# Kernel tuning notes

Measured on AMD Instinct MI355X. Metric: run time of the kernel, lower is better.

## Reference

```python
import jax, jax.numpy as jnp
import numpy as np

H = 40  # HIDDEN_SIZE


def _gru_layer(x_tbi, Wih, Whh, bih, bhh):
    """PyTorch-convention GRU layer. x_tbi: (T, B, I). Returns (ys (T,B,H), h_T (B,H)).
    Gate order in stacked weights is (r, z, n) as in torch.nn.GRU:
      r = sigmoid(W_ir x + b_ir + W_hr h + b_hr)
      z = sigmoid(W_iz x + b_iz + W_hz h + b_hz)
      n = tanh(W_in x + b_in + r * (W_hn h + b_hn))
      h' = (1 - z) * n + z * h
    """
    # Precompute all input projections in one big GEMM: (T,B,3H)
    xg = jnp.einsum('tbi,gi->tbg', x_tbi, Wih) + bih
    B = x_tbi.shape[1]
    h0 = jnp.zeros((B, H), x_tbi.dtype)

    def step(h, xg_t):
        hg = h @ Whh.T + bhh                       # (B, 3H)
        xr, xz, xn = jnp.split(xg_t, 3, axis=-1)
        hr, hz, hn = jnp.split(hg, 3, axis=-1)
        r = jax.nn.sigmoid(xr + hr)
        z = jax.nn.sigmoid(xz + hz)
        n = jnp.tanh(xn + r * hn)
        h_new = (1.0 - z) * n + z * h
        return h_new, h_new

    hT, ys = jax.lax.scan(step, h0, xg)
    return ys, hT


def setup_inputs() -> dict:
    key = jax.random.key(0)
    ks = jax.random.split(key, 9)
    B, T, I = 4096, 256, 16
    s = 1.0 / np.sqrt(H)  # torch GRU init: U(-1/sqrt(H), 1/sqrt(H))
    u = lambda k, shape: jax.random.uniform(k, shape, jnp.float32, -s, s)
    return {
        "x": jax.random.normal(ks[0], (B, T, I), jnp.float32),
        "Wih0": u(ks[1], (3 * H, I)),
        "Whh0": u(ks[2], (3 * H, H)),
        "bih0": u(ks[3], (3 * H,)),
        "bhh0": u(ks[4], (3 * H,)),
        "Wih1": u(ks[5], (3 * H, H)),
        "Whh1": u(ks[6], (3 * H, H)),
        "bih1": u(ks[7], (3 * H,)),
        "bhh1": u(ks[8], (3 * H,)),
    }


def reference(x, Wih0, Whh0, bih0, bhh0, Wih1, Whh1, bih1, bhh1):
    # batch_first input (B,T,I) -> time-major (T,B,I) for scan
    x_tbi = jnp.transpose(x, (1, 0, 2))
    y0, _ = _gru_layer(x_tbi, Wih0, Whh0, bih0, bhh0)   # layer 0 full sequence
    _, hT = _gru_layer(y0, Wih1, Whh1, bih1, bhh1)      # layer 1 final state
    return hT  # (B, H) == h[-1]
```

## Files before the change

kernel.cpp:

```cpp
#include <hip/hip_runtime.h>

#define T_STEPS 256
#define HID 40
#define EPB 16
#define NTHR 640
#define RR 56
#define PP (16 * RR)
#define OL1 (2 * PP)
#define STOT (4 * PP)

typedef __attribute__((ext_vector_type(8))) short bf16x8;
typedef __attribute__((ext_vector_type(4))) float f32x4;
typedef __attribute__((ext_vector_type(8))) float f32x8;
typedef __attribute__((ext_vector_type(4))) unsigned int u32x4;

__device__ __forceinline__ unsigned short bf16_rne(float v) {
    unsigned int x = __float_as_uint(v);
    unsigned int r = x + 0x7FFFu + ((x >> 16) & 1u);
    return (unsigned short)(r >> 16);
}
__device__ __forceinline__ unsigned short bf16_cvt(float v) {
    unsigned int r;
    asm("v_cvt_pk_bf16_f32 %0, %1, %2" : "=v"(r) : "v"(v), "v"(v));
    return (unsigned short)r;
}
__device__ __forceinline__ float sigm(float v) {
    return __builtin_amdgcn_rcpf(1.0f + __builtin_amdgcn_exp2f(-1.4426950408889634f * v));
}
__device__ __forceinline__ float tanh_f(float v) {
    return 1.0f - 2.0f * __builtin_amdgcn_rcpf(__builtin_amdgcn_exp2f(2.8853900817779268f * v) + 1.0f);
}

#define MF(A_, B_, C_) C_ = __builtin_amdgcn_mfma_f32_16x16x32_bf16(A_, B_, C_, 0, 0, 0)
#define PINV(v) asm volatile("" : "+v"(v))

__device__ bf16x8 afrag(const float* Whh, const float* Wih, int KX,
                        int rh, int rx, int c, int qrow) {
    bf16x8 f;
    #pragma unroll
    for (int j = 0; j < 8; ++j) f[j] = 0;
    #pragma unroll
    for (int j = 0; j < 8; ++j) {
        const int k = 32 * c + qrow * 8 + j;
        if (k < 40) {
            if (rh >= 0) f[j] = (short)bf16_rne(Whh[rh * 40 + k]);
        } else if (k < 40 + KX) {
            if (rx >= 0) f[j] = (short)bf16_rne(Wih[rx * KX + (k - 40)]);
        }
    }
    return f;
}

__global__ __launch_bounds__(NTHR, 1)
void gru2_kernel(const float* __restrict__ x,
                 const float* __restrict__ Wih0, const float* __restrict__ Whh0,
                 const float* __restrict__ bih0, const float* __restrict__ bhh0,
                 const float* __restrict__ Wih1, const float* __restrict__ Whh1,
                 const float* __restrict__ bih1, const float* __restrict__ bhh1,
                 float* __restrict__ out)
{
    __shared__ __align__(16) unsigned short S[STOT];

    const int tid  = threadIdx.x;
    const int wid  = tid >> 6;
    const int l    = tid & 63;
    const int col  = l & 15;
    const int qrow = l >> 4;
    const int ps   = (l & 15) & 3;
    const int pu   = (l & 15) >> 2;
    const int e0   = blockIdx.x * EPB;

    const bool isL1 = wid >= 5;
    const int  m    = isL1 ? wid - 5 : wid;

    const float* Whh = isL1 ? Whh1 : Whh0;
    const float* Wih = isL1 ? Wih1 : Wih0;
    const float* bih = isL1 ? bih1 : bih0;
    const float* bhh = isL1 ? bhh1 : bhh0;
    const int KX = isL1 ? 40 : 16;

    bf16x8 ZF;
    #pragma unroll
    for (int j = 0; j < 8; ++j) ZF[j] = 0;
    bf16x8 F00=ZF,F01=ZF,F02=ZF, F10=ZF,F11=ZF,F12=ZF;
    f32x4 BB0, BB1;
    {
#define RRX(u, RH, RX) \
        const int RH = (ps == 2) ? -1 : (ps == 0 ? (u) : ps == 1 ? 40 + (u) : 80 + (u)); \
        const int RX = (ps == 3) ? -1 : (ps == 0 ? (u) : ps == 1 ? 40 + (u) : 80 + (u));
        {
            const int u0 = 4 * (2 * m) + pu;
            RRX(u0, rh0, rx0);
            F00 = afrag(Whh, Wih, KX, rh0, rx0, 0, qrow);
            F01 = afrag(Whh, Wih, KX, rh0, rx0, 1, qrow);
            if (isL1) F02 = afrag(Whh, Wih, KX, rh0, rx0, 2, qrow);
        }
        {
            const int u1 = 4 * (2 * m + 1) + pu;
            RRX(u1, rh1, rx1);
            F10 = afrag(Whh, Wih, KX, rh1, rx1, 0, qrow);
            F11 = afrag(Whh, Wih, KX, rh1, rx1, 1, qrow);
            if (isL1) F12 = afrag(Whh, Wih, KX, rh1, rx1, 2, qrow);
        }
        const int uc0 = 8 * m + qrow;
        const int uc1 = 8 * m + 4 + qrow;
        BB0[0] = bih[uc0] + bhh[uc0];
        BB0[1] = bih[40 + uc0] + bhh[40 + uc0];
        BB0[2] = bih[80 + uc0];
        BB0[3] = bhh[80 + uc0];
        BB1[0] = bih[uc1] + bhh[uc1];
        BB1[1] = bih[40 + uc1] + bhh[40 + uc1];
        BB1[2] = bih[80 + uc1];
        BB1[3] = bhh[80 + uc1];
    }
    PINV(F00); PINV(F01); PINV(F02);
    PINV(F10); PINV(F11); PINV(F12);
    PINV(BB0); PINV(BB1);

    int rd0, rd1, g0, g1, g2;
    rd0 = col * RR + 8 * qrow;
    rd1 = col * RR + 32;
    {
        auto ga = [&](int g) -> int {
            if (g < 5)  return OL1 + col * RR + 8 * g;
            if (g < 10) return col * RR + 8 * (g - 5);
            return col * RR;
        };
        g0 = ga(qrow);
        g1 = ga(4 + qrow);
        g2 = ga(8 + qrow);
    }
    const int w0  = col * RR + 8 * m + qrow;
    const int w0b = w0 + 4;
    const int w1  = OL1 + col * RR + 8 * m + qrow;
    const int w1b = w1 + 4;
    const bool usex = (qrow == 1) || (qrow == 2);
    unsigned short* Sb = &S[0];
    float hA0 = 0.f, hA1 = 0.f;
    f32x4 cP0, cP1;
    cP0[0]=cP0[1]=cP0[2]=cP0[3]=0.f;
    cP1[0]=cP1[1]=cP1[2]=cP1[3]=0.f;

    for (int idx = tid; idx < STOT; idx += NTHR) Sb[idx] = 0;

    const float* xrow = x + (size_t)(e0 + col) * (T_STEPS * 16) + ((qrow == 2) ? 8 : 0);
    f32x8 XA, XB;
    #pragma unroll
    for (int j = 0; j < 8; ++j) { XA[j] = 0.f; XB[j] = 0.f; }
    if (!isL1) {
        XA = *(const f32x8*)(xrow);
        XB = *(const f32x8*)(xrow + 16);
    }
    __syncthreads();

#define GMATH(C, H) \
    const float r_ = sigm(C[0]); \
    const float z_ = sigm(C[1]); \
    const float n_ = tanh_f(C[2] + r_ * C[3]); \
    H = n_ + z_ * (H - n_);

#define STEP(RP, XQ) { \
     \
    if (!isL1) { \
        const bf16x8 S0 = *(const bf16x8*)(Sb + rd0 + (RP) * PP); \
        bf16x8 S1 = *(const bf16x8*)(Sb + rd1 + (RP) * PP); \
        unsigned int xw0, xw1, xw2, xw3; \
        asm("v_cvt_pk_bf16_f32 %0, %1, %2" : "=v"(xw0) : "v"(XQ[0]), "v"(XQ[1])); \
        asm("v_cvt_pk_bf16_f32 %0, %1, %2" : "=v"(xw1) : "v"(XQ[2]), "v"(XQ[3])); \
        asm("v_cvt_pk_bf16_f32 %0, %1, %2" : "=v"(xw2) : "v"(XQ[4]), "v"(XQ[5])); \
        asm("v_cvt_pk_bf16_f32 %0, %1, %2" : "=v"(xw3) : "v"(XQ[6]), "v"(XQ[7])); \
        if (t + 2 < T_STEPS) XQ = *(const f32x8*)(xrow + (t + 2) * 16); \
        u32x4 s1u = *(const u32x4*)&S1; \
        s1u[0] = usex ? xw0 : s1u[0]; \
        s1u[1] = usex ? xw1 : s1u[1]; \
        s1u[2] = usex ? xw2 : s1u[2]; \
        s1u[3] = usex ? xw3 : s1u[3]; \
        S1 = *(const bf16x8*)&s1u; \
        cA0 = __builtin_amdgcn_mfma_f32_16x16x32_bf16(F00, S0, BB0, 0, 0, 0); \
        MF(F01, S1, cA0); \
        cA1 = __builtin_amdgcn_mfma_f32_16x16x32_bf16(F10, S0, BB1, 0, 0, 0); \
        MF(F11, S1, cA1); \
    } else if (t >= 2) { \
        { GMATH(cP0, hA0); Sb[w1  + (RP) * PP] = bf16_cvt(hA0); } \
        { GMATH(cP1, hA1); Sb[w1b + (RP) * PP] = bf16_cvt(hA1); } \
    } \
    __syncthreads();   \
     \
    if (!isL1) { \
        { GMATH(cA0, hA0); Sb[w0  + (1 - (RP)) * PP] = bf16_cvt(hA0); } \
        { GMATH(cA1, hA1); Sb[w0b + (1 - (RP)) * PP] = bf16_cvt(hA1); } \
    } else { \
        const bf16x8 S0 = *(const bf16x8*)(Sb + g0 + (RP) * PP); \
        const bf16x8 S1 = *(const bf16x8*)(Sb + g1 + (RP) * PP); \
        const bf16x8 S2 = *(const bf16x8*)(Sb + g2 + (RP) * PP); \
        cP0 = __builtin_amdgcn_mfma_f32_16x16x32_bf16(F00, S0, BB0, 0, 0, 0); \
        MF(F01, S1, cP0); MF(F02, S2, cP0); \
        cP1 = __builtin_amdgcn_mfma_f32_16x16x32_bf16(F10, S0, BB1, 0, 0, 0); \
        MF(F11, S1, cP1); MF(F12, S2, cP1); \
    } \
    ++t; \
    __syncthreads();   }

    int t = 0;
    f32x4 cA0, cA1;
    #pragma unroll 1
    for (int it = 0; it < 128; ++it) {
        STEP(0, XA)
        STEP(1, XB)
    }

    if (isL1) {
        { GMATH(cP0, hA0); Sb[w1  + 0 * PP] = bf16_cvt(hA0); }
        { GMATH(cP1, hA1); Sb[w1b + 0 * PP] = bf16_cvt(hA1); }
    }
    __syncthreads();
    if (isL1) {
        const bf16x8 S0 = *(const bf16x8*)(Sb + g0 + 0 * PP);
        const bf16x8 S1 = *(const bf16x8*)(Sb + g1 + 0 * PP);
        const bf16x8 S2 = *(const bf16x8*)(Sb + g2 + 0 * PP);
        f32x4 c0 = __builtin_amdgcn_mfma_f32_16x16x32_bf16(F00, S0, BB0, 0, 0, 0);
        MF(F01, S1, c0); MF(F02, S2, c0);
        f32x4 c1 = __builtin_amdgcn_mfma_f32_16x16x32_bf16(F10, S0, BB1, 0, 0, 0);
        MF(F11, S1, c1); MF(F12, S2, c1);
        { GMATH(c0, hA0); }
        { GMATH(c1, hA1); }
        float* op = out + (size_t)(e0 + col) * HID + 8 * m + qrow;
        op[0] = hA0;
        op[4] = hA1;
    }
}

extern "C" void kernel_launch(void* const* d_in, const int* in_sizes, int n_in,
                              void* d_out, int out_size, void* d_ws, size_t ws_size,
                              hipStream_t stream) {
    const float* x    = (const float*)d_in[0];
    const float* Wih0 = (const float*)d_in[1];
    const float* Whh0 = (const float*)d_in[2];
    const float* bih0 = (const float*)d_in[3];
    const float* bhh0 = (const float*)d_in[4];
    const float* Wih1 = (const float*)d_in[5];
    const float* Whh1 = (const float*)d_in[6];
    const float* bih1 = (const float*)d_in[7];
    const float* bhh1 = (const float*)d_in[8];
    float* out = (float*)d_out;

    dim3 grid(4096 / EPB), block(NTHR);
    hipLaunchKernelGGL(gru2_kernel, grid, block, 0, stream,
                       x, Wih0, Whh0, bih0, bhh0, Wih1, Whh1, bih1, bhh1, out);
}
```

Baseline: 239.0 us.

## Rebalance GRU waves to 16 per block with one barrier per step

Raises the block from 10 to 16 waves. Layer-1 work is spread over 10 waves with one 4-unit tile each, and layer-0 over 6 waves, four with two tiles and two with one. Each step now does its MFMA, gate math and h write in the same phase, so a single barrier per timestep replaces the previous two. The barrier is a custom lgkmcnt wait plus s_barrier wrapped in sched_barriers, and the x prefetch distance grows to four steps. The aim is less serialization and barrier overhead per step. In exchange, the layer-0 waves are unevenly loaded and the tighter launch bounds put more pressure on registers.

Measured after the change: 234.9 us. No clear change (-1.7%).

```diff
diff --git a/kernel.cpp b/kernel.cpp
--- a/kernel.cpp
+++ b/kernel.cpp
@@ -3,7 +3,7 @@
 #define T_STEPS 256
 #define HID 40
 #define EPB 16
-#define NTHR 640
+#define NTHR 1024
 #define RR 56
 #define PP (16 * RR)
 #define OL1 (2 * PP)
@@ -33,6 +33,12 @@
 
 #define MF(A_, B_, C_) C_ = __builtin_amdgcn_mfma_f32_16x16x32_bf16(A_, B_, C_, 0, 0, 0)
 #define PINV(v) asm volatile("" : "+v"(v))
+
+#define BAR() do { \
+    __builtin_amdgcn_sched_barrier(0); \
+    asm volatile("s_waitcnt lgkmcnt(0)\n\ts_barrier" ::: "memory"); \
+    __builtin_amdgcn_sched_barrier(0); \
+} while (0)
 
 __device__ bf16x8 afrag(const float* Whh, const float* Wih, int KX,
                         int rh, int rx, int c, int qrow) {
@@ -51,7 +57,7 @@
     return f;
 }
 
-__global__ __launch_bounds__(NTHR, 1)
+__global__ __launch_bounds__(NTHR, 4)
 void gru2_kernel(const float* __restrict__ x,
                  const float* __restrict__ Wih0, const float* __restrict__ Whh0,
                  const float* __restrict__ bih0, const float* __restrict__ bhh0,
@@ -70,8 +76,11 @@
     const int pu   = (l & 15) >> 2;
     const int e0   = blockIdx.x * EPB;
 
-    const bool isL1 = wid >= 5;
-    const int  m    = isL1 ? wid - 5 : wid;
+    const bool isL1 = wid >= 6;
+    const int  NT   = (!isL1 && wid < 4) ? 2 : 1;
+    const int  TA   = isL1 ? (wid - 6) : (wid < 4 ? 2 * wid : wid + 4);
+    const int  TB   = (NT == 2) ? TA + 1 : TA;
+    const bool dB   = (NT != 2);
 
     const float* Whh = isL1 ? Whh1 : Whh0;
     const float* Wih = isL1 ? Wih1 : Wih0;
@@ -82,44 +91,43 @@
     bf16x8 ZF;
     #pragma unroll
     for (int j = 0; j < 8; ++j) ZF[j] = 0;
-    bf16x8 F00=ZF,F01=ZF,F02=ZF, F10=ZF,F11=ZF,F12=ZF;
+    bf16x8 F00=ZF,F01=ZF,F02=ZF, F10=ZF,F11=ZF;
     f32x4 BB0, BB1;
     {
 #define RRX(u, RH, RX) \
         const int RH = (ps == 2) ? -1 : (ps == 0 ? (u) : ps == 1 ? 40 + (u) : 80 + (u)); \
         const int RX = (ps == 3) ? -1 : (ps == 0 ? (u) : ps == 1 ? 40 + (u) : 80 + (u));
         {
-            const int u0 = 4 * (2 * m) + pu;
+            const int u0 = 4 * TA + pu;
             RRX(u0, rh0, rx0);
             F00 = afrag(Whh, Wih, KX, rh0, rx0, 0, qrow);
             F01 = afrag(Whh, Wih, KX, rh0, rx0, 1, qrow);
             if (isL1) F02 = afrag(Whh, Wih, KX, rh0, rx0, 2, qrow);
         }
-        {
-            const int u1 = 4 * (2 * m + 1) + pu;
+        if (NT == 2) {
+            const int u1 = 4 * TB + pu;
             RRX(u1, rh1, rx1);
             F10 = afrag(Whh, Wih, KX, rh1, rx1, 0, qrow);
             F11 = afrag(Whh, Wih, KX, rh1, rx1, 1, qrow);
-            if (isL1) F12 = afrag(Whh, Wih, KX, rh1, rx1, 2, qrow);
         }
-        const int uc0 = 8 * m + qrow;
-        const int uc1 = 8 * m + 4 + qrow;
+        const int uc0 = 4 * TA + qrow;
+        const int uc1 = 4 * TB + qrow;
         BB0[0] = bih[uc0] + bhh[uc0];
         BB0[1] = bih[40 + uc0] + bhh[40 + uc0];
         BB0[2] = bih[80 + uc0];
         BB0[3] = bhh[80 + uc0];
-        BB1[0] = bih[uc1] + bhh[uc1];
-        BB1[1] = bih[40 + uc1] + bhh[40 + uc1];
-        BB1[2] = bih[80 + uc1];
-        BB1[3] = bhh[80 + uc1];
+        BB1[0] = dB ? 0.f : (bih[uc1] + bhh[uc1]);
+        BB1[1] = dB ? 0.f : (bih[40 + uc1] + bhh[40 + uc1]);
+        BB1[2] = dB ? 0.f : bih[80 + uc1];
+        BB1[3] = dB ? 0.f : bhh[80 + uc1];
     }
     PINV(F00); PINV(F01); PINV(F02);
-    PINV(F10); PINV(F11); PINV(F12);
+    PINV(F10); PINV(F11);
     PINV(BB0); PINV(BB1);
 
-    int rd0, rd1, g0, g1, g2;
-    rd0 = col * RR + 8 * qrow;
-    rd1 = col * RR + 32;
+    const int rd0 = col * RR + 8 * qrow;
+    const int rd1 = col * RR + 32;
+    int g0, g1, g2;
     {
         auto ga = [&](int g) -> int {
             if (g < 5)  return OL1 + col * RR + 8 * g;
@@ -130,26 +138,24 @@
         g1 = ga(4 + qrow);
         g2 = ga(8 + qrow);
     }
-    const int w0  = col * RR + 8 * m + qrow;
-    const int w0b = w0 + 4;
-    const int w1  = OL1 + col * RR + 8 * m + qrow;
-    const int w1b = w1 + 4;
+    const int w0  = col * RR + 4 * TA + qrow;
+    const int w0b = col * RR + 4 * TB + qrow;
+    const int w1  = OL1 + col * RR + 4 * TA + qrow;
     const bool usex = (qrow == 1) || (qrow == 2);
     unsigned short* Sb = &S[0];
     float hA0 = 0.f, hA1 = 0.f;
-    f32x4 cP0, cP1;
-    cP0[0]=cP0[1]=cP0[2]=cP0[3]=0.f;
-    cP1[0]=cP1[1]=cP1[2]=cP1[3]=0.f;
 
     for (int idx = tid; idx < STOT; idx += NTHR) Sb[idx] = 0;
 
     const float* xrow = x + (size_t)(e0 + col) * (T_STEPS * 16) + ((qrow == 2) ? 8 : 0);
-    f32x8 XA, XB;
-    #pragma unroll
-    for (int j = 0; j < 8; ++j) { XA[j] = 0.f; XB[j] = 0.f; }
+    f32x8 XA, XB, XC, XD;
+    #pragma unroll
+    for (int j = 0; j < 8; ++j) { XA[j] = 0.f; XB[j] = 0.f; XC[j] = 0.f; XD[j] = 0.f; }
     if (!isL1) {
         XA = *(const f32x8*)(xrow);
         XB = *(const f32x8*)(xrow + 16);
+        XC = *(const f32x8*)(xrow + 32);
+        XD = *(const f32x8*)(xrow + 48);
     }
     __syncthreads();
 
@@ -159,74 +165,55 @@
     const float n_ = tanh_f(C[2] + r_ * C[3]); \
     H = n_ + z_ * (H - n_);
 
-#define STEP(RP, XQ) { \
-     \
+#define BODY(RP, XQ) { \
     if (!isL1) { \
-        const bf16x8 S0 = *(const bf16x8*)(Sb + rd0 + (RP) * PP); \
-        bf16x8 S1 = *(const bf16x8*)(Sb + rd1 + (RP) * PP); \
-        unsigned int xw0, xw1, xw2, xw3; \
-        asm("v_cvt_pk_bf16_f32 %0, %1, %2" : "=v"(xw0) : "v"(XQ[0]), "v"(XQ[1])); \
-        asm("v_cvt_pk_bf16_f32 %0, %1, %2" : "=v"(xw1) : "v"(XQ[2]), "v"(XQ[3])); \
-        asm("v_cvt_pk_bf16_f32 %0, %1, %2" : "=v"(xw2) : "v"(XQ[4]), "v"(XQ[5])); \
-        asm("v_cvt_pk_bf16_f32 %0, %1, %2" : "=v"(xw3) : "v"(XQ[6]), "v"(XQ[7])); \
-        if (t + 2 < T_STEPS) XQ = *(const f32x8*)(xrow + (t + 2) * 16); \
-        u32x4 s1u = *(const u32x4*)&S1; \
-        s1u[0] = usex ? xw0 : s1u[0]; \
-        s1u[1] = usex ? xw1 : s1u[1]; \
-        s1u[2] = usex ? xw2 : s1u[2]; \
-        s1u[3] = usex ? xw3 : s1u[3]; \
-        S1 = *(const bf16x8*)&s1u; \
-        cA0 = __builtin_amdgcn_mfma_f32_16x16x32_bf16(F00, S0, BB0, 0, 0, 0); \
-        MF(F01, S1, cA0); \
-        cA1 = __builtin_amdgcn_mfma_f32_16x16x32_bf16(F10, S0, BB1, 0, 0, 0); \
-        MF(F11, S1, cA1); \
-    } else if (t >= 2) { \
-        { GMATH(cP0, hA0); Sb[w1  + (RP) * PP] = bf16_cvt(hA0); } \
-        { GMATH(cP1, hA1); Sb[w1b + (RP) * PP] = bf16_cvt(hA1); } \
-    } \
-    __syncthreads();   \
-     \
-    if (!isL1) { \
-        { GMATH(cA0, hA0); Sb[w0  + (1 - (RP)) * PP] = bf16_cvt(hA0); } \
-        { GMATH(cA1, hA1); Sb[w0b + (1 - (RP)) * PP] = bf16_cvt(hA1); } \
+        if (t < T_STEPS) { \
+            const bf16x8 S0 = *(const bf16x8*)(Sb + rd0 + (RP) * PP); \
+            bf16x8 S1 = *(const bf16x8*)(Sb + rd1 + (RP) * PP); \
+            unsigned int xw0, xw1, xw2, xw3; \
+            asm("v_cvt_pk_bf16_f32 %0, %1, %2" : "=v"(xw0) : "v"(XQ[0]), "v"(XQ[1])); \
+            asm("v_cvt_pk_bf16_f32 %0, %1, %2" : "=v"(xw1) : "v"(XQ[2]), "v"(XQ[3])); \
+            asm("v_cvt_pk_bf16_f32 %0, %1, %2" : "=v"(xw2) : "v"(XQ[4]), "v"(XQ[5])); \
+            asm("v_cvt_pk_bf16_f32 %0, %1, %2" : "=v"(xw3) : "v"(XQ[6]), "v"(XQ[7])); \
+            if (t + 4 < T_STEPS) XQ = *(const f32x8*)(xrow + (t + 4) * 16); \
+            u32x4 s1u = *(const u32x4*)&S1; \
+            s1u[0] = usex ? xw0 : s1u[0]; \
+            s1u[1] = usex ? xw1 : s1u[1]; \
+            s1u[2] = usex ? xw2 : s1u[2]; \
+            s1u[3] = usex ? xw3 : s1u[3]; \
+            S1 = *(const bf16x8*)&s1u; \
+            f32x4 c0 = __builtin_amdgcn_mfma_f32_16x16x32_bf16(F00, S0, BB0, 0, 0, 0); \
+            MF(F01, S1, c0); \
+            { GMATH(c0, hA0); Sb[w0 + (1 - (RP)) * PP] = bf16_cvt(hA0); } \
+            if (NT == 2) { \
+                f32x4 c1 = __builtin_amdgcn_mfma_f32_16x16x32_bf16(F10, S0, BB1, 0, 0, 0); \
+                MF(F11, S1, c1); \
+                GMATH(c1, hA1); Sb[w0b + (1 - (RP)) * PP] = bf16_cvt(hA1); \
+            } \
+        } \
     } else { \
         const bf16x8 S0 = *(const bf16x8*)(Sb + g0 + (RP) * PP); \
         const bf16x8 S1 = *(const bf16x8*)(Sb + g1 + (RP) * PP); \
         const bf16x8 S2 = *(const bf16x8*)(Sb + g2 + (RP) * PP); \
-        cP0 = __builtin_amdgcn_mfma_f32_16x16x32_bf16(F00, S0, BB0, 0, 0, 0); \
-        MF(F01, S1, cP0); MF(F02, S2, cP0); \
-        cP1 = __builtin_amdgcn_mfma_f32_16x16x32_bf16(F10, S0, BB1, 0, 0, 0); \
-        MF(F11, S1, cP1); MF(F12, S2, cP1); \
+        f32x4 c = __builtin_amdgcn_mfma_f32_16x16x32_bf16(F00, S0, BB0, 0, 0, 0); \
+        MF(F01, S1, c); MF(F02, S2, c); \
+        if (t > 0) { GMATH(c, hA0); Sb[w1 + (1 - (RP)) * PP] = bf16_cvt(hA0); } \
     } \
     ++t; \
-    __syncthreads();   }
+    BAR(); }
 
     int t = 0;
-    f32x4 cA0, cA1;
     #pragma unroll 1
-    for (int it = 0; it < 128; ++it) {
-        STEP(0, XA)
-        STEP(1, XB)
-    }
+    for (int it = 0; it < 64; ++it) {
+        BODY(0, XA)
+        BODY(1, XB)
+        BODY(0, XC)
+        BODY(1, XD)
+    }
+    BODY(0, XA)
 
     if (isL1) {
-        { GMATH(cP0, hA0); Sb[w1  + 0 * PP] = bf16_cvt(hA0); }
-        { GMATH(cP1, hA1); Sb[w1b + 0 * PP] = bf16_cvt(hA1); }
-    }
-    __syncthreads();
-    if (isL1) {
-        const bf16x8 S0 = *(const bf16x8*)(Sb + g0 + 0 * PP);
-        const bf16x8 S1 = *(const bf16x8*)(Sb + g1 + 0 * PP);
-        const bf16x8 S2 = *(const bf16x8*)(Sb + g2 + 0 * PP);
-        f32x4 c0 = __builtin_amdgcn_mfma_f32_16x16x32_bf16(F00, S0, BB0, 0, 0, 0);
-        MF(F01, S1, c0); MF(F02, S2, c0);
-        f32x4 c1 = __builtin_amdgcn_mfma_f32_16x16x32_bf16(F10, S0, BB1, 0, 0, 0);
-        MF(F11, S1, c1); MF(F12, S2, c1);
-        { GMATH(c0, hA0); }
-        { GMATH(c1, hA1); }
-        float* op = out + (size_t)(e0 + col) * HID + 8 * m + qrow;
-        op[0] = hA0;
-        op[4] = hA1;
+        out[(size_t)(e0 + col) * HID + 4 * TA + qrow] = hA0;
     }
 }
 
```
